# Kernel optimization log

Measured on AMD Instinct MI355X. Metric: run time of the kernel, lower is better.

The kernel has to match this reference:

```python
import jax, jax.numpy as jnp
import numpy as np

N, E, IN, ED, H, C, G, NC = 50000, 800000, 128, 32, 4, 16, 64, 2
HC = H * C  # 64
NEG_SLOPE = 0.2
EPS = 1e-5


def _layernorm(x, g, b):
    mu = jnp.mean(x, axis=-1, keepdims=True)
    var = jnp.mean((x - mu) ** 2, axis=-1, keepdims=True)
    return (x - mu) * jax.lax.rsqrt(var + EPS) * g + b


def _gat(x, src, dst, edge_attr, W, a_src, a_dst, We, a_edge, b):
    """PyG GATConv (v1) with edge features, concat=True."""
    n = x.shape[0]
    h, c = a_src.shape
    xw = (x @ W).reshape(n, h, c)                       # [N,H,C]
    al_src = jnp.sum(xw * a_src, axis=-1)               # [N,H]
    al_dst = jnp.sum(xw * a_dst, axis=-1)               # [N,H]
    ew = (edge_attr @ We).reshape(-1, h, c)             # [Ef,H,C]
    al_e = jnp.sum(ew * a_edge, axis=-1)                # [Ef,H]
    alpha = al_src[src] + al_dst[dst] + al_e            # [Ef,H]
    alpha = jnp.where(alpha > 0, alpha, NEG_SLOPE * alpha)
    # segment softmax over incoming edges of each dst node
    amax = jax.ops.segment_max(alpha, dst, num_segments=n)
    amax = jnp.where(jnp.isfinite(amax), amax, 0.0)
    ex = jnp.exp(alpha - amax[dst])
    denom = jax.ops.segment_sum(ex, dst, num_segments=n)
    att = ex / (denom[dst] + 1e-16)                     # [Ef,H]
    msg = xw[src] * att[:, :, None]                     # [Ef,H,C]
    out = jax.ops.segment_sum(msg, dst, num_segments=n) # [N,H,C]
    return out.reshape(n, h * c) + b


def setup_inputs() -> dict:
    ks = jax.random.split(jax.random.key(0), 24)
    s = 0.1
    inp = {
        "x": jax.random.normal(ks[0], (N, IN), jnp.float32),
        "edge_attr": jax.random.normal(ks[1], (E, ED), jnp.float32),
        "W1": jax.random.normal(ks[2], (IN, HC), jnp.float32) * s,
        "as1": jax.random.normal(ks[3], (H, C), jnp.float32) * s,
        "ad1": jax.random.normal(ks[4], (H, C), jnp.float32) * s,
        "We1": jax.random.normal(ks[5], (ED, HC), jnp.float32) * s,
        "ae1": jax.random.normal(ks[6], (H, C), jnp.float32) * s,
        "b1": jnp.zeros((HC,), jnp.float32),
        "W2": jax.random.normal(ks[7], (HC, HC), jnp.float32) * s,
        "as2": jax.random.normal(ks[8], (H, C), jnp.float32) * s,
        "ad2": jax.random.normal(ks[9], (H, C), jnp.float32) * s,
        "We2": jax.random.normal(ks[10], (ED, HC), jnp.float32) * s,
        "ae2": jax.random.normal(ks[11], (H, C), jnp.float32) * s,
        "b2": jnp.zeros((HC,), jnp.float32),
        "g1": jnp.ones((HC,), jnp.float32),
        "be1": jnp.zeros((HC,), jnp.float32),
        "fw1": jax.random.normal(ks[12], (HC, 32), jnp.float32) * s,
        "fb1": jnp.zeros((32,), jnp.float32),
        "g2": jnp.ones((32,), jnp.float32),
        "be2": jnp.zeros((32,), jnp.float32),
        "fw2": jax.random.normal(ks[13], (32, NC), jnp.float32) * s,
        "fb2": jnp.zeros((NC,), jnp.float32),
        "edge_index": jax.random.randint(ks[14], (2, E), 0, N, jnp.int64),
        "batch": jnp.sort(jax.random.randint(ks[15], (N,), 0, G, jnp.int64)),
    }
    return inp


def reference(x, edge_attr, W1, as1, ad1, We1, ae1, b1, W2, as2, ad2, We2, ae2,
              b2, g1, be1, fw1, fb1, g2, be2, fw2, fb2, edge_index, batch):
    src, dst = edge_index[0], edge_index[1]
    e = edge_attr.shape[0]
    # add_self_loops with fill_value='mean' (mean of incoming edge_attr per node)
    cnt = jax.ops.segment_sum(jnp.ones((e,), x.dtype), dst, num_segments=N)
    loop_ea = jax.ops.segment_sum(edge_attr, dst, num_segments=N) / jnp.clip(cnt, 1.0)[:, None]
    ar = jnp.arange(N)
    src_f = jnp.concatenate([src, ar])
    dst_f = jnp.concatenate([dst, ar])
    ea_f = jnp.concatenate([edge_attr, loop_ea], axis=0)

    h = _gat(x, src_f, dst_f, ea_f, W1, as1, ad1, We1, ae1, b1)
    h = jax.nn.relu(h)
    h = _layernorm(h, g1, be1)
    h = _gat(h, src_f, dst_f, ea_f, W2, as2, ad2, We2, ae2, b2)
    h = jax.nn.relu(h)
    pooled = jax.ops.segment_max(h, batch, num_segments=G)   # global_max_pool
    pooled = jnp.where(jnp.isfinite(pooled), pooled, 0.0)
    z = pooled @ fw1 + fb1
    z = _layernorm(z, g2, be2)
    z = jax.nn.relu(z)
    # dropout(p=0.4) is identity in eval mode
    z = z @ fw2 + fb2
    return jax.nn.log_softmax(z, axis=1)
```

## Files before the change

### kernel.cpp

```cpp
#include <hip/hip_runtime.h>
#include <math.h>

#define N_NODES 50000
#define N_EDGES 800000
#define IN_DIM 128
#define ED_DIM 32
#define NH 4
#define CH 16
#define HC 64
#define NG 64
#define NCL 2
#define NEG_SLOPE 0.2f
#define LN_EPS 1e-5f
#define NBLK1 196
#define NB_TILE 3125
#define NB_ECH 3125

__global__ void k_scan_local(const int* __restrict__ cnt, int* __restrict__ tmp_ex,
                             int* __restrict__ bsum) {
    __shared__ int sd[256];
    int t = threadIdx.x, idx = blockIdx.x * 256 + t;
    int v = (idx < N_NODES) ? cnt[idx] : 0;
    sd[t] = v; __syncthreads();
    for (int off = 1; off < 256; off <<= 1) {
        int add = (t >= off) ? sd[t - off] : 0;
        __syncthreads();
        sd[t] += add;
        __syncthreads();
    }
    if (idx < N_NODES) tmp_ex[idx] = sd[t] - v;
    if (t == 255) bsum[blockIdx.x] = sd[t];
}

__global__ __launch_bounds__(256) void k_phase1(
        const float* __restrict__ X, const float* __restrict__ W,
        const float* __restrict__ AS, const float* __restrict__ AD,
        float* __restrict__ XW, float* __restrict__ ALS, float* __restrict__ ALD,
        const float* __restrict__ ea,
        const float* __restrict__ We1, const float* __restrict__ ae1,
        const float* __restrict__ We2, const float* __restrict__ ae2,
        float4* __restrict__ ale8,
        const int* __restrict__ dst, int* __restrict__ cnt, int* __restrict__ rank_e) {
    __shared__ float smem[IN_DIM * HC + 16 * IN_DIM];
    int job = blockIdx.x % 3;
    int bid = blockIdx.x / 3;
    int t = threadIdx.x;
    if (job == 0) {
        const int K = IN_DIM;
        float* sW = smem;
        float* sX = smem + K * HC;
        for (int i = t; i < K * HC; i += 256) sW[i] = W[i];
        int nb = bid * 16;
        for (int i = t; i < 16 * K; i += 256) sX[i] = X[(long long)nb * K + i];
        __syncthreads();
        int sub = t >> 6, j = t & 63;
        float acc[4] = {0.f, 0.f, 0.f, 0.f};
        #pragma unroll 8
        for (int k = 0; k < K; ++k) {
            float wv = sW[k * HC + j];
            #pragma unroll
            for (int q = 0; q < 4; ++q) acc[q] += sX[(sub + 4 * q) * K + k] * wv;
        }
        float as_ = AS[j], ad_ = AD[j];
        #pragma unroll
        for (int q = 0; q < 4; ++q) {
            int n = nb + sub + 4 * q;
            XW[(long long)n * HC + j] = acc[q];
            float vs = acc[q] * as_, vd = acc[q] * ad_;
            #pragma unroll
            for (int m = 1; m < 16; m <<= 1) { vs += __shfl_xor(vs, m); vd += __shfl_xor(vd, m); }
            if ((j & 15) == 0) {
                int h = j >> 4;
                ALS[n * 4 + h] = vs; ALD[n * 4 + h] = vd;
            }
        }
    } else if (job == 1) {
        float* sVe = smem;
        {
            int d = t >> 3, k = t & 7;
            int l = k >> 2, h = k & 3;
            const float* We = l ? We2 : We1;
            const float* ae = l ? ae2 : ae1;
            float s = 0.f;
            #pragma unroll
            for (int c = 0; c < CH; ++c) s += We[d * HC + h * CH + c] * ae[h * CH + c];
            sVe[d * 8 + k] = s;
        }
        __syncthreads();
        int e = bid * 256 + t;
        if (e >= N_EDGES) return;
        float a[8];
        #pragma unroll
        for (int k = 0; k < 8; ++k) a[k] = 0.f;
        const float4* er4 = (const float4*)(ea + (long long)e * ED_DIM);
        #pragma unroll
        for (int q = 0; q < ED_DIM / 4; ++q) {
            float4 v = er4[q];
            float ev[4] = {v.x, v.y, v.z, v.w};
            #pragma unroll
            for (int u = 0; u < 4; ++u) {
                #pragma unroll
                for (int k = 0; k < 8; ++k) a[k] += ev[u] * sVe[(q * 4 + u) * 8 + k];
            }
        }
        float4* out = ale8 + (long long)e * 2;
        out[0] = make_float4(a[0], a[1], a[2], a[3]);
        out[1] = make_float4(a[4], a[5], a[6], a[7]);
    } else {
        int e = bid * 256 + t;
        if (e < N_EDGES) rank_e[e] = atomicAdd(&cnt[dst[e]], 1);
    }
}

__global__ void k_scan_perm(const int* __restrict__ tmp_ex, const int* __restrict__ bsum,
                            int* __restrict__ row_start,
                            const int* __restrict__ dst, const int* __restrict__ srcI,
                            const int* __restrict__ rank_e, int2* __restrict__ perm_src) {
    __shared__ int sd[256];
    __shared__ int sboff[256];
    int t = threadIdx.x;
    int v = (t < NBLK1) ? bsum[t] : 0;
    sd[t] = v; __syncthreads();
    for (int off = 1; off < 256; off <<= 1) {
        int add = (t >= off) ? sd[t - off] : 0;
        __syncthreads();
        sd[t] += add;
        __syncthreads();
    }
    sboff[t] = sd[t] - v;
    __syncthreads();
    if (blockIdx.x < NBLK1) {
        int idx = blockIdx.x * 256 + t;
        if (idx < N_NODES) row_start[idx] = tmp_ex[idx] + sboff[blockIdx.x];
        if (idx == 0) row_start[N_NODES] = N_EDGES;
    } else {
        int e = (blockIdx.x - NBLK1) * 256 + t;
        if (e < N_EDGES) {
            int d = dst[e];
            int pos = tmp_ex[d] + sboff[d >> 8] + rank_e[e];
            perm_src[pos] = make_int2(e, srcI[e]);
        }
    }
}

__global__ void k_agg1x(const int* __restrict__ rs, const int2* __restrict__ ps,
                        const float* __restrict__ ale8,
                        const float* __restrict__ ALS, const float* __restrict__ ALD,
                        const float* __restrict__ XW, const float* __restrict__ bias,
                        const float* __restrict__ gam, const float* __restrict__ bet,
                        const float* __restrict__ W2,
                        const float* __restrict__ AS2, const float* __restrict__ AD2,
                        float* __restrict__ XW2, float* __restrict__ ALS2,
                        float* __restrict__ ALD2) {
    __shared__ float sh[4][HC];
    int wid = threadIdx.x >> 6;
    int n = (blockIdx.x * blockDim.x + threadIdx.x) >> 6;
    if (n >= N_NODES) return;
    int lane = threadIdx.x & 63;
    int h = lane >> 4;
    int e0 = rs[n], e1 = rs[n + 1];
    float adn = ALD[n * 4 + h];
    float acc0 = 0.f, l0 = 0.f, as0 = 0.f;
    float acc1 = 0.f, l1 = 0.f, as1 = 0.f;
    float acc2 = 0.f, l2 = 0.f, as2 = 0.f;
    float acc3 = 0.f, l3 = 0.f, as3 = 0.f;
    int e = e0;
    for (; e + 3 < e1; e += 4) {
        int2 pA = ps[e], pB = ps[e + 1], pC = ps[e + 2], pD = ps[e + 3];
        float aeA = ale8[(long long)pA.x * 8 + h];
        float aeB = ale8[(long long)pB.x * 8 + h];
        float aeC = ale8[(long long)pC.x * 8 + h];
        float aeD = ale8[(long long)pD.x * 8 + h];
        float xA = XW[pA.y * HC + lane];
        float xB = XW[pB.y * HC + lane];
        float xC = XW[pC.y * HC + lane];
        float xD = XW[pD.y * HC + lane];
        float aA = ALS[pA.y * 4 + h] + adn + aeA;
        float aB = ALS[pB.y * 4 + h] + adn + aeB;
        float aC = ALS[pC.y * 4 + h] + adn + aeC;
        float aD = ALS[pD.y * 4 + h] + adn + aeD;
        aA = aA > 0.f ? aA : NEG_SLOPE * aA;
        aB = aB > 0.f ? aB : NEG_SLOPE * aB;
        aC = aC > 0.f ? aC : NEG_SLOPE * aC;
        aD = aD > 0.f ? aD : NEG_SLOPE * aD;
        float qA = __expf(aA), qB = __expf(aB), qC = __expf(aC), qD = __expf(aD);
        acc0 += qA * xA; l0 += qA; as0 += aeA;
        acc1 += qB * xB; l1 += qB; as1 += aeB;
        acc2 += qC * xC; l2 += qC; as2 += aeC;
        acc3 += qD * xD; l3 += qD; as3 += aeD;
    }
    for (; e < e1; ++e) {
        int2 pA = ps[e];
        float aeA = ale8[(long long)pA.x * 8 + h];
        float xA = XW[pA.y * HC + lane];
        float aA = ALS[pA.y * 4 + h] + adn + aeA;
        aA = aA > 0.f ? aA : NEG_SLOPE * aA;
        float qA = __expf(aA);
        acc0 += qA * xA; l0 += qA; as0 += aeA;
    }
    int d = e1 - e0;
    float invd = 1.f / (float)(d > 0 ? d : 1);
    float aSelf = ALS[n * 4 + h] + adn + (as0 + as1 + as2 + as3) * invd;
    aSelf = aSelf > 0.f ? aSelf : NEG_SLOPE * aSelf;
    float pS = __expf(aSelf);
    float acc = (acc0 + acc1) + (acc2 + acc3) + pS * XW[n * HC + lane];
    float l = (l0 + l1) + (l2 + l3) + pS;
    float v = acc / (l + 1e-16f) + bias[lane];
    v = fmaxf(v, 0.f);
    {
        float s1 = v;
        #pragma unroll
        for (int mm = 1; mm < 64; mm <<= 1) s1 += __shfl_xor(s1, mm);
        float mean = s1 * (1.f / 64.f);
        float dd = v - mean;
        float s2 = dd * dd;
        #pragma unroll
        for (int mm = 1; mm < 64; mm <<= 1) s2 += __shfl_xor(s2, mm);
        float var = s2 * (1.f / 64.f);
        v = dd * rsqrtf(var + LN_EPS) * gam[lane] + bet[lane];
    }
    sh[wid][lane] = v;
    __syncthreads();
    float a2 = 0.f;
    #pragma unroll 8
    for (int k = 0; k < HC; ++k) {
        a2 += sh[wid][k] * W2[k * HC + lane];
    }
    XW2[(long long)n * HC + lane] = a2;
    float vs = a2 * AS2[lane], vd = a2 * AD2[lane];
    #pragma unroll
    for (int m = 1; m < 16; m <<= 1) { vs += __shfl_xor(vs, m); vd += __shfl_xor(vd, m); }
    if ((lane & 15) == 0) {
        ALS2[n * 4 + h] = vs; ALD2[n * 4 + h] = vd;
    }
}

__global__ void k_agg2p(const int* __restrict__ rs, const int2* __restrict__ ps,
                        const float* __restrict__ ale8,
                        const float* __restrict__ ALS, const float* __restrict__ ALD,
                        const float* __restrict__ XW, const float* __restrict__ bias,
                        const int* __restrict__ batch, float* __restrict__ pooled) {
    int n = (blockIdx.x * blockDim.x + threadIdx.x) >> 6;
    if (n >= N_NODES) return;
    int lane = threadIdx.x & 63;
    int h = lane >> 4;
    int e0 = rs[n], e1 = rs[n + 1];
    float adn = ALD[n * 4 + h];
    float acc0 = 0.f, l0 = 0.f, as0 = 0.f;
    float acc1 = 0.f, l1 = 0.f, as1 = 0.f;
    float acc2 = 0.f, l2 = 0.f, as2 = 0.f;
    float acc3 = 0.f, l3 = 0.f, as3 = 0.f;
    int e = e0;
    for (; e + 3 < e1; e += 4) {
        int2 pA = ps[e], pB = ps[e + 1], pC = ps[e + 2], pD = ps[e + 3];
        float aeA = ale8[(long long)pA.x * 8 + 4 + h];
        float aeB = ale8[(long long)pB.x * 8 + 4 + h];
        float aeC = ale8[(long long)pC.x * 8 + 4 + h];
        float aeD = ale8[(long long)pD.x * 8 + 4 + h];
        float xA = XW[pA.y * HC + lane];
        float xB = XW[pB.y * HC + lane];
        float xC = XW[pC.y * HC + lane];
        float xD = XW[pD.y * HC + lane];
        float aA = ALS[pA.y * 4 + h] + adn + aeA;
        float aB = ALS[pB.y * 4 + h] + adn + aeB;
        float aC = ALS[pC.y * 4 + h] + adn + aeC;
        float aD = ALS[pD.y * 4 + h] + adn + aeD;
        aA = aA > 0.f ? aA : NEG_SLOPE * aA;
        aB = aB > 0.f ? aB : NEG_SLOPE * aB;
        aC = aC > 0.f ? aC : NEG_SLOPE * aC;
        aD = aD > 0.f ? aD : NEG_SLOPE * aD;
        float qA = __expf(aA), qB = __expf(aB), qC = __expf(aC), qD = __expf(aD);
        acc0 += qA * xA; l0 += qA; as0 += aeA;
        acc1 += qB * xB; l1 += qB; as1 += aeB;
        acc2 += qC * xC; l2 += qC; as2 += aeC;
        acc3 += qD * xD; l3 += qD; as3 += aeD;
    }
    for (; e < e1; ++e) {
        int2 pA = ps[e];
        float aeA = ale8[(long long)pA.x * 8 + 4 + h];
        float xA = XW[pA.y * HC + lane];
        float aA = ALS[pA.y * 4 + h] + adn + aeA;
        aA = aA > 0.f ? aA : NEG_SLOPE * aA;
        float qA = __expf(aA);
        acc0 += qA * xA; l0 += qA; as0 += aeA;
    }
    int d = e1 - e0;
    float invd = 1.f / (float)(d > 0 ? d : 1);
    float aSelf = ALS[n * 4 + h] + adn + (as0 + as1 + as2 + as3) * invd;
    aSelf = aSelf > 0.f ? aSelf : NEG_SLOPE * aSelf;
    float pS = __expf(aSelf);
    float acc = (acc0 + acc1) + (acc2 + acc3) + pS * XW[n * HC + lane];
    float l = (l0 + l1) + (l2 + l3) + pS;
    float v = acc / (l + 1e-16f) + bias[lane];
    v = fmaxf(v, 0.f);
    int g = batch[n];
    atomicMax((unsigned int*)&pooled[g * HC + lane], __float_as_uint(v));
}

__global__ void k_head(const float* __restrict__ pooled,
                       const float* __restrict__ fw1, const float* __restrict__ fb1,
                       const float* __restrict__ g2, const float* __restrict__ be2,
                       const float* __restrict__ fw2, const float* __restrict__ fb2,
                       float* __restrict__ out) {
    int g = blockIdx.x;
    int j = threadIdx.x;
    float z = 0.f;
    if (j < 32) {
        for (int k = 0; k < HC; ++k) z += pooled[g * HC + k] * fw1[k * 32 + j];
        z += fb1[j];
    }
    float s1 = (j < 32) ? z : 0.f;
    for (int m = 1; m < 32; m <<= 1) s1 += __shfl_xor(s1, m, 32);
    float mean = s1 * (1.f / 32.f);
    float d = z - mean;
    float s2 = (j < 32) ? d * d : 0.f;
    for (int m = 1; m < 32; m <<= 1) s2 += __shfl_xor(s2, m, 32);
    float var = s2 * (1.f / 32.f);
    float zz = 0.f;
    if (j < 32) {
        zz = d * rsqrtf(var + LN_EPS) * g2[j] + be2[j];
        zz = fmaxf(zz, 0.f);
    }
    float p0 = (j < 32) ? zz * fw2[j * NCL + 0] : 0.f;
    float p1 = (j < 32) ? zz * fw2[j * NCL + 1] : 0.f;
    for (int m = 1; m < 32; m <<= 1) { p0 += __shfl_xor(p0, m, 32); p1 += __shfl_xor(p1, m, 32); }
    if (j == 0) {
        float l0 = p0 + fb2[0], l1 = p1 + fb2[1];
        float mx = fmaxf(l0, l1);
        float ls = mx + logf(__expf(l0 - mx) + __expf(l1 - mx));
        out[g * NCL + 0] = l0 - ls;
        out[g * NCL + 1] = l1 - ls;
    }
}

extern "C" void kernel_launch(void* const* d_in, const int* in_sizes, int n_in,
                              void* d_out, int out_size, void* d_ws, size_t ws_size,
                              hipStream_t stream) {
    const float* x   = (const float*)d_in[0];
    const float* ea  = (const float*)d_in[1];
    const float* W1  = (const float*)d_in[2];
    const float* as1 = (const float*)d_in[3];
    const float* ad1 = (const float*)d_in[4];
    const float* We1 = (const float*)d_in[5];
    const float* ae1 = (const float*)d_in[6];
    const float* b1  = (const float*)d_in[7];
    const float* W2  = (const float*)d_in[8];
    const float* as2 = (const float*)d_in[9];
    const float* ad2 = (const float*)d_in[10];
    const float* We2 = (const float*)d_in[11];
    const float* ae2 = (const float*)d_in[12];
    const float* b2  = (const float*)d_in[13];
    const float* g1  = (const float*)d_in[14];
    const float* be1 = (const float*)d_in[15];
    const float* fw1 = (const float*)d_in[16];
    const float* fb1 = (const float*)d_in[17];
    const float* g2  = (const float*)d_in[18];
    const float* be2 = (const float*)d_in[19];
    const float* fw2 = (const float*)d_in[20];
    const float* fb2 = (const float*)d_in[21];
    const int* eidx  = (const int*)d_in[22];
    const int* batch = (const int*)d_in[23];
    const int* srcI = eidx;
    const int* dstI = eidx + N_EDGES;

    char* w = (char*)d_ws;
    auto alloc = [&](size_t bytes) { char* p = w; w += (bytes + 255) & ~(size_t)255; return p; };
    int*   cnt       = (int*)  alloc((size_t)N_NODES * 4);
    int*   row_start = (int*)  alloc((size_t)(N_NODES + 1) * 4);
    int*   rank_e    = (int*)  alloc((size_t)N_EDGES * 4);
    int*   tmp_ex    = (int*)  alloc((size_t)N_NODES * 4);
    int*   bsum      = (int*)  alloc(256 * 4);
    int2*  perm_src  = (int2*) alloc((size_t)N_EDGES * 8);
    float4* ale8     = (float4*)alloc((size_t)N_EDGES * 32);
    float* xw1       = (float*)alloc((size_t)N_NODES * HC * 4);
    float* als1      = (float*)alloc((size_t)N_NODES * 4 * 4);
    float* ald1      = (float*)alloc((size_t)N_NODES * 4 * 4);
    float* xw2       = (float*)alloc((size_t)N_NODES * HC * 4);
    float* als2      = (float*)alloc((size_t)N_NODES * 4 * 4);
    float* ald2      = (float*)alloc((size_t)N_NODES * 4 * 4);
    float* pooled    = (float*)alloc((size_t)NG * HC * 4);

    hipMemsetAsync(cnt, 0, (size_t)N_NODES * 4, stream);
    hipMemsetAsync(pooled, 0, (size_t)NG * HC * 4, stream);

    k_phase1<<<3 * NB_TILE, 256, 0, stream>>>(x, W1, as1, ad1, xw1, als1, ald1,
                                              ea, We1, ae1, We2, ae2, ale8,
                                              dstI, cnt, rank_e);
    k_scan_local<<<NBLK1, 256, 0, stream>>>(cnt, tmp_ex, bsum);
    k_scan_perm<<<NBLK1 + NB_ECH, 256, 0, stream>>>(tmp_ex, bsum, row_start,
                                                    dstI, srcI, rank_e, perm_src);

    k_agg1x<<<N_NODES / 4, 256, 0, stream>>>(row_start, perm_src, (const float*)ale8,
                                             als1, ald1, xw1, b1, g1, be1,
                                             W2, as2, ad2, xw2, als2, ald2);
    k_agg2p<<<N_NODES / 4, 256, 0, stream>>>(row_start, perm_src, (const float*)ale8,
                                             als2, ald2, xw2, b2, batch, pooled);

    k_head<<<NG, 64, 0, stream>>>(pooled, fw1, fb1, g2, be2, fw2, fb2, (float*)d_out);
}
```

Baseline: 435.4 us.

## Stage edge attrs via shared memory, cache W2 in LDS, split pooling into separate kernel

The edge-logit job now loads each block's edge_attr tile cooperatively into padded shared memory with coalesced float4 reads, instead of a per-thread strided row read. k_agg1x copies W2 into shared memory once per block and drops the per-node global W2 reads. The second aggregation no longer does one atomicMax per node; it writes h2 to a buffer, and a new k_pool kernel does a running max over contiguous nodes per graph before issuing atomics. This cuts atomic contention but adds an extra 12.8MB write and read plus one more kernel launch.

```diff
diff --git a/kernel.cpp b/kernel.cpp
--- a/kernel.cpp
+++ b/kernel.cpp
@@ -76,6 +76,7 @@
         }
     } else if (job == 1) {
         float* sVe = smem;
+        float* sE  = smem + 256;
         {
             int d = t >> 3, k = t & 7;
             int l = k >> 2, h = k & 3;
@@ -86,21 +87,29 @@
             for (int c = 0; c < CH; ++c) s += We[d * HC + h * CH + c] * ae[h * CH + c];
             sVe[d * 8 + k] = s;
         }
+        {
+            const float4* gsrc = (const float4*)ea + (size_t)bid * 2048;
+            #pragma unroll
+            for (int r = 0; r < 8; ++r) {
+                int i4 = t + r * 256;
+                float4 v = gsrc[i4];
+                float* dp = sE + (i4 >> 3) * 33 + ((i4 & 7) << 2);
+                dp[0] = v.x; dp[1] = v.y; dp[2] = v.z; dp[3] = v.w;
+            }
+        }
         __syncthreads();
         int e = bid * 256 + t;
-        if (e >= N_EDGES) return;
         float a[8];
         #pragma unroll
         for (int k = 0; k < 8; ++k) a[k] = 0.f;
-        const float4* er4 = (const float4*)(ea + (long long)e * ED_DIM);
+        const float* row = sE + t * 33;
         #pragma unroll
         for (int q = 0; q < ED_DIM / 4; ++q) {
-            float4 v = er4[q];
-            float ev[4] = {v.x, v.y, v.z, v.w};
             #pragma unroll
             for (int u = 0; u < 4; ++u) {
+                float ev = row[q * 4 + u];
                 #pragma unroll
-                for (int k = 0; k < 8; ++k) a[k] += ev[u] * sVe[(q * 4 + u) * 8 + k];
+                for (int k = 0; k < 8; ++k) a[k] += ev * sVe[(q * 4 + u) * 8 + k];
             }
         }
         float4* out = ale8 + (long long)e * 2;
@@ -143,20 +152,23 @@
     }
 }
 
-__global__ void k_agg1x(const int* __restrict__ rs, const int2* __restrict__ ps,
-                        const float* __restrict__ ale8,
-                        const float* __restrict__ ALS, const float* __restrict__ ALD,
-                        const float* __restrict__ XW, const float* __restrict__ bias,
-                        const float* __restrict__ gam, const float* __restrict__ bet,
-                        const float* __restrict__ W2,
-                        const float* __restrict__ AS2, const float* __restrict__ AD2,
-                        float* __restrict__ XW2, float* __restrict__ ALS2,
-                        float* __restrict__ ALD2) {
+__global__ __launch_bounds__(256) void k_agg1x(
+        const int* __restrict__ rs, const int2* __restrict__ ps,
+        const float* __restrict__ ale8,
+        const float* __restrict__ ALS, const float* __restrict__ ALD,
+        const float* __restrict__ XW, const float* __restrict__ bias,
+        const float* __restrict__ gam, const float* __restrict__ bet,
+        const float* __restrict__ W2,
+        const float* __restrict__ AS2, const float* __restrict__ AD2,
+        float* __restrict__ XW2, float* __restrict__ ALS2, float* __restrict__ ALD2) {
+    __shared__ float sW2[HC * HC];
     __shared__ float sh[4][HC];
-    int wid = threadIdx.x >> 6;
-    int n = (blockIdx.x * blockDim.x + threadIdx.x) >> 6;
-    if (n >= N_NODES) return;
-    int lane = threadIdx.x & 63;
+    int t = threadIdx.x;
+    for (int i = t; i < HC * HC; i += 256) sW2[i] = W2[i];
+    __syncthreads();
+    int wid = t >> 6;
+    int n = blockIdx.x * 4 + wid;
+    int lane = t & 63;
     int h = lane >> 4;
     int e0 = rs[n], e1 = rs[n + 1];
     float adn = ALD[n * 4 + h];
@@ -220,12 +232,9 @@
         v = dd * rsqrtf(var + LN_EPS) * gam[lane] + bet[lane];
     }
     sh[wid][lane] = v;
-    __syncthreads();
     float a2 = 0.f;
     #pragma unroll 8
-    for (int k = 0; k < HC; ++k) {
-        a2 += sh[wid][k] * W2[k * HC + lane];
-    }
+    for (int k = 0; k < HC; ++k) a2 += sh[wid][k] * sW2[k * HC + lane];
     XW2[(long long)n * HC + lane] = a2;
     float vs = a2 * AS2[lane], vd = a2 * AD2[lane];
     #pragma unroll
@@ -235,11 +244,13 @@
     }
 }
 
-__global__ void k_agg2p(const int* __restrict__ rs, const int2* __restrict__ ps,
-                        const float* __restrict__ ale8,
-                        const float* __restrict__ ALS, const float* __restrict__ ALD,
-                        const float* __restrict__ XW, const float* __restrict__ bias,
-                        const int* __restrict__ batch, float* __restrict__ pooled) {
+template<bool DO_LN, int LOFF>
+__global__ void k_agg(const int* __restrict__ rs, const int2* __restrict__ ps,
+                      const float* __restrict__ ale8,
+                      const float* __restrict__ ALS, const float* __restrict__ ALD,
+                      const float* __restrict__ XW, const float* __restrict__ bias,
+                      const float* __restrict__ gam, const float* __restrict__ bet,
+                      float* __restrict__ OUT) {
     int n = (blockIdx.x * blockDim.x + threadIdx.x) >> 6;
     if (n >= N_NODES) return;
     int lane = threadIdx.x & 63;
@@ -253,10 +264,10 @@
     int e = e0;
     for (; e + 3 < e1; e += 4) {
         int2 pA = ps[e], pB = ps[e + 1], pC = ps[e + 2], pD = ps[e + 3];
-        float aeA = ale8[(long long)pA.x * 8 + 4 + h];
-        float aeB = ale8[(long long)pB.x * 8 + 4 + h];
-        float aeC = ale8[(long long)pC.x * 8 + 4 + h];
-        float aeD = ale8[(long long)pD.x * 8 + 4 + h];
+        float aeA = ale8[(long long)pA.x * 8 + LOFF + h];
+        float aeB = ale8[(long long)pB.x * 8 + LOFF + h];
+        float aeC = ale8[(long long)pC.x * 8 + LOFF + h];
+        float aeD = ale8[(long long)pD.x * 8 + LOFF + h];
         float xA = XW[pA.y * HC + lane];
         float xB = XW[pB.y * HC + lane];
         float xC = XW[pC.y * HC + lane];
@@ -277,7 +288,7 @@
     }
     for (; e < e1; ++e) {
         int2 pA = ps[e];
-        float aeA = ale8[(long long)pA.x * 8 + 4 + h];
+        float aeA = ale8[(long long)pA.x * 8 + LOFF + h];
         float xA = XW[pA.y * HC + lane];
         float aA = ALS[pA.y * 4 + h] + adn + aeA;
         aA = aA > 0.f ? aA : NEG_SLOPE * aA;
@@ -293,8 +304,36 @@
     float l = (l0 + l1) + (l2 + l3) + pS;
     float v = acc / (l + 1e-16f) + bias[lane];
     v = fmaxf(v, 0.f);
-    int g = batch[n];
-    atomicMax((unsigned int*)&pooled[g * HC + lane], __float_as_uint(v));
+    if (DO_LN) {
+        float s1 = v;
+        #pragma unroll
+        for (int mm = 1; mm < 64; mm <<= 1) s1 += __shfl_xor(s1, mm);
+        float mean = s1 * (1.f / 64.f);
+        float dd = v - mean;
+        float s2 = dd * dd;
+        #pragma unroll
+        for (int mm = 1; mm < 64; mm <<= 1) s2 += __shfl_xor(s2, mm);
+        float var = s2 * (1.f / 64.f);
+        v = dd * rsqrtf(var + LN_EPS) * gam[lane] + bet[lane];
+    }
+    OUT[(long long)n * HC + lane] = v;
+}
+
+__global__ void k_pool(const float* __restrict__ H2, const int* __restrict__ batch,
+                       float* __restrict__ pooled) {
+    int j = threadIdx.x & 63;
+    int r = threadIdx.x >> 6;
+    int base = blockIdx.x * 128;
+    int gcur = -1; float rm = 0.f;
+    for (int n = base + r; n < base + 128 && n < N_NODES; n += 4) {
+        int g = batch[n];
+        if (g != gcur) {
+            if (gcur >= 0) atomicMax((unsigned int*)&pooled[gcur * HC + j], __float_as_uint(rm));
+            gcur = g; rm = 0.f;
+        }
+        rm = fmaxf(rm, H2[(long long)n * HC + j]);
+    }
+    if (gcur >= 0) atomicMax((unsigned int*)&pooled[gcur * HC + j], __float_as_uint(rm));
 }
 
 __global__ void k_head(const float* __restrict__ pooled,
@@ -378,6 +417,7 @@
     float* xw2       = (float*)alloc((size_t)N_NODES * HC * 4);
     float* als2      = (float*)alloc((size_t)N_NODES * 4 * 4);
     float* ald2      = (float*)alloc((size_t)N_NODES * 4 * 4);
+    float* h2        = (float*)alloc((size_t)N_NODES * HC * 4);
     float* pooled    = (float*)alloc((size_t)NG * HC * 4);
 
     hipMemsetAsync(cnt, 0, (size_t)N_NODES * 4, stream);
@@ -393,8 +433,9 @@
     k_agg1x<<<N_NODES / 4, 256, 0, stream>>>(row_start, perm_src, (const float*)ale8,
                                              als1, ald1, xw1, b1, g1, be1,
                                              W2, as2, ad2, xw2, als2, ald2);
-    k_agg2p<<<N_NODES / 4, 256, 0, stream>>>(row_start, perm_src, (const float*)ale8,
-                                             als2, ald2, xw2, b2, batch, pooled);
-
+    k_agg<false, 4><<<N_NODES / 4, 256, 0, stream>>>(row_start, perm_src, (const float*)ale8,
+                                                     als2, ald2, xw2, b2, nullptr, nullptr, h2);
+
+    k_pool<<<(N_NODES + 127) / 128, 256, 0, stream>>>(h2, batch, pooled);
     k_head<<<NG, 64, 0, stream>>>(pooled, fw1, fb1, g2, be2, fw2, fb2, (float*)d_out);
 }
```

Result: faster. 409.6 us (-5.9%).
